# Performance work log

Hardware: AMD Instinct MI355X
Metric: run time of the kernel (lower is better)

Reference implementation:

```python
import jax, jax.numpy as jnp
import numpy as np

B, T, I, H, NSHIFT = 64, 1024, 128, 512, 32


def setup_inputs() -> dict:
    key = jax.random.key(0)
    ks = jax.random.split(key, 8)
    s_in = 1.0 / np.sqrt(I)
    s_h = 1.0 / np.sqrt(H)
    return {
        "x": jax.random.normal(ks[0], (B, T, I), dtype=jnp.float32),
        "W1": jax.random.uniform(ks[1], (I, H), minval=-s_in, maxval=s_in, dtype=jnp.float32),
        "b1": jax.random.uniform(ks[2], (H,), minval=-s_in, maxval=s_in, dtype=jnp.float32),
        "W_ih": jax.random.uniform(ks[3], (H, 4 * H), minval=-s_h, maxval=s_h, dtype=jnp.float32),
        "W_hh": jax.random.uniform(ks[4], (H, 4 * H), minval=-s_h, maxval=s_h, dtype=jnp.float32),
        "b_lstm": jax.random.uniform(ks[5], (4 * H,), minval=-s_h, maxval=s_h, dtype=jnp.float32),
        "Wo": jax.random.uniform(ks[6], (H, NSHIFT), minval=-s_h, maxval=s_h, dtype=jnp.float32),
        "bo": jax.random.uniform(ks[7], (NSHIFT,), minval=-s_h, maxval=s_h, dtype=jnp.float32),
    }


def _lstm_scan(xs, W_ih, W_hh, b, hidden):
    # xs: [T, B, H] (time-major for scan). Sine activation replaces tanh.
    Bsz = xs.shape[1]
    h0 = jnp.zeros((Bsz, hidden), dtype=xs.dtype)
    c0 = jnp.zeros((Bsz, hidden), dtype=xs.dtype)

    def step(carry, xt):
        h, c = carry
        gates = xt @ W_ih + h @ W_hh + b  # [B, 4H]
        i, f, g, o = jnp.split(gates, 4, axis=-1)
        i = jax.nn.sigmoid(i)
        f = jax.nn.sigmoid(f)
        g = jnp.sin(g)  # sine activation in place of tanh
        o = jax.nn.sigmoid(o)
        c_new = f * c + i * g
        h_new = o * jnp.sin(c_new)
        return (h_new, c_new), h_new

    (hT, cT), hs = jax.lax.scan(step, (h0, c0), xs)
    return hs, (hT, cT)


def reference(x, W1, b1, W_ih, W_hh, b_lstm, Wo, bo):
    # fc1: [B, T, I] -> [B, T, H]
    fc1_out = x @ W1 + b1
    xs = jnp.swapaxes(fc1_out, 0, 1)  # [T, B, H]
    hs, _ = _lstm_scan(xs, W_ih, W_hh, b_lstm, W_hh.shape[0])
    lstm_out = jnp.swapaxes(hs, 0, 1)  # [B, T, H]
    return lstm_out @ Wo + bo  # [B, T, n_shift]
```

## Files before the change

kernel.cpp:

```cpp
#include <hip/hip_runtime.h>


constexpr int Bb = 64;
constexpr int Tt = 1024;
constexpr int Ii = 128;
constexpr int Hh = 512;
constexpr int G4 = 2048;
constexpr int NS = 32;
constexpr int NG = 16;
constexpr int GW = 16;
constexpr int BPG = 4;

typedef _Float16 h2 __attribute__((ext_vector_type(2)));
typedef _Float16 h8 __attribute__((ext_vector_type(8)));
typedef float    f4 __attribute__((ext_vector_type(4)));
typedef unsigned int u32;
typedef u32 u32x2 __attribute__((ext_vector_type(2)));
typedef u32 u32x4 __attribute__((ext_vector_type(4)));

__device__ __forceinline__ float dot8(h8 w, h8 x, float acc) {
  h2 w0 = {w[0], w[1]}, w1 = {w[2], w[3]}, w2 = {w[4], w[5]}, w3 = {w[6], w[7]};
  h2 x0 = {x[0], x[1]}, x1 = {x[2], x[3]}, x2 = {x[4], x[5]}, x3 = {x[6], x[7]};
  acc = __builtin_amdgcn_fdot2(x0, w0, acc, false);
  acc = __builtin_amdgcn_fdot2(x1, w1, acc, false);
  acc = __builtin_amdgcn_fdot2(x2, w2, acc, false);
  acc = __builtin_amdgcn_fdot2(x3, w3, acc, false);
  return acc;
}

__device__ __forceinline__ float sigf(float x) { return 1.f / (1.f + __expf(-x)); }


__global__ void k_wc(const float* __restrict__ W1, const float* __restrict__ Wih,
                     const float* __restrict__ b1, const float* __restrict__ bl,
                     _Float16* __restrict__ Wc4, float* __restrict__ bias2) {
  const int j = blockIdx.x;
  const int i = threadIdx.x;
  __shared__ float col[Hh];
  __shared__ float part[128];
  for (int k = i; k < Hh; k += 128) col[k] = Wih[k * G4 + j];
  __syncthreads();
  float s = 0.f;
  for (int k = i; k < Hh; k += 128) s += b1[k] * col[k];
  part[i] = s;
  __syncthreads();
  if (i == 0) {
    float t = bl[j];
    for (int k = 0; k < 128; k++) t += part[k];
    bias2[j] = t;
  }
  float acc = 0.f;
  const float* w1r = W1 + i * Hh;
#pragma unroll 4
  for (int k = 0; k < Hh; k++) acc += w1r[k] * col[k];
  const int gate = j >> 9, r = j & 511, ss = r >> 5, u = r & 31;
  const int c128 = gate * 32 + u, cb = c128 >> 4, c = c128 & 15;
  const int lane = ((i >> 3) & 3) * 16 + c, ks4 = i >> 5, e = i & 7;
  Wc4[((ss * 8 + cb) * 4 + ks4) * 512 + lane * 8 + e] = (_Float16)acc;
}

__global__ void k_whh(const float* __restrict__ W, _Float16* __restrict__ W4) {
  const int id = blockIdx.x * 256 + threadIdx.x;
  const int lane = id & 63, ks = (id >> 6) & 15, cb = (id >> 10) & 7, ss = id >> 13;
  const int c = lane & 15, c128 = cb * 16 + c;
  const int gate = c128 >> 5, u = c128 & 31;
  const int colg = gate * 512 + ss * 32 + u;
  h8 o;
#pragma unroll
  for (int e = 0; e < 8; ++e)
    o[e] = (_Float16)W[(ks * 32 + (lane >> 4) * 8 + e) * G4 + colg];
  *(h8*)(W4 + ((ss * 8 + cb) * 16 + ks) * 512 + lane * 8) = o;
}

__global__ __launch_bounds__(512, 1) void k_scan(
    const float* __restrict__ x, const _Float16* __restrict__ Wc4,
    const float* __restrict__ bias2, const _Float16* __restrict__ Whh4,
    const float* __restrict__ Wo, const float* __restrict__ bo,
    float* __restrict__ out, char* __restrict__ hpub) {
  const int gid = blockIdx.x >> 4, ss = blockIdx.x & 15;
  const int tid = threadIdx.x;
  const int lane = tid & 63, wv = tid >> 6;
  const int l15 = lane & 15, l4 = lane >> 4;

  __shared__ __align__(16) char hls[2][16384];
  __shared__ __align__(16) char xws[4096];
  __shared__ __align__(16) char wots[32768];
  __shared__ float pre_s[2][2][4][4][33];
  __shared__ float gat_s[4][4][33];
  __shared__ float op_s[32][17];

  h8 bW[16], bC[4];
#pragma unroll
  for (int ks = 0; ks < 16; ++ks)
    bW[ks] = *(const h8*)(Whh4 + ((ss * 8 + wv) * 16 + ks) * 512 + lane * 8);
#pragma unroll
  for (int ks = 0; ks < 4; ++ks)
    bC[ks] = *(const h8*)(Wc4 + ((ss * 8 + wv) * 4 + ks) * 512 + lane * 8);

  const int b8 = tid >> 5, ml = tid & 31;
  const float bI = bias2[ss * 32 + ml],        bF = bias2[512 + ss * 32 + ml],
              bG = bias2[1024 + ss * 32 + ml], bO = bias2[1536 + ss * 32 + ml];
  const int nn = tid & 31, pp = tid >> 5;
  const float bor = (tid < NS) ? bo[tid] : 0.f;

#pragma unroll
  for (int q = 0; q < 2; ++q) {
    u32x4 z = {0, 0, 0, 0};
    *(u32x4*)(hls[0] + (q * 512 + tid) * 16) = z;
    *(u32x4*)(hls[1] + (q * 512 + tid) * 16) = z;
  }
  if (tid < 256) { u32x4 z = {0, 0, 0, 0}; *(u32x4*)(xws + tid * 16) = z; }
  for (int it = tid; it < Hh * NS; it += 512) {
    int k = it >> 5, n = it & 31;
    *(_Float16*)(wots + n * 1024 + ((2 * k) ^ ((n & 7) << 4))) = (_Float16)Wo[k * NS + n];
  }
  float c_ = 0.f;

  auto stage_x = [&](int t0) {
    if (tid < 128) {
      const int row = tid >> 4, cc = tid & 15;
      const float* src = x + ((size_t)(gid * BPG + (row & 3)) * Tt + t0 + (row >> 2)) * Ii + cc * 8;
      f4 s0 = *(const f4*)src, s1 = *(const f4*)(src + 4);
      h8 v = {(_Float16)s0[0], (_Float16)s0[1], (_Float16)s0[2], (_Float16)s0[3],
              (_Float16)s1[0], (_Float16)s1[1], (_Float16)s1[2], (_Float16)s1[3]};
      *(h8*)(xws + row * 256 + ((cc * 16) ^ ((row & 7) << 4))) = v;
    }
  };
  auto do_pregate = [&](int buf) {
    f4 pa = {0.f, 0.f, 0.f, 0.f};
#pragma unroll
    for (int ks = 0; ks < 4; ++ks) {
      const int row = l15;
      h8 a = *(const h8*)(xws + row * 256 + ((ks * 64 + l4 * 16) ^ ((row & 7) << 4)));
      pa = __builtin_amdgcn_mfma_f32_16x16x32_f16(a, bC[ks], pa, 0, 0, 0);
    }
    if (l4 < 2) {
      const int c128 = wv * 16 + l15, gam = c128 >> 5, u = c128 & 31;
#pragma unroll
      for (int e = 0; e < 4; ++e) {
        const int row = l4 * 4 + e;
        pre_s[buf][row >> 2][row & 3][gam][u] = pa[e];
      }
    }
  };
  auto op_part = [&](const char* hb) {
    if (ss < BPG) {
      float acc = 0.f;
#pragma unroll
      for (int q = 0; q < 4; ++q) {
        h8 w_ = *(const h8*)(wots + nn * 1024 + ((pp * 64 + q * 16) ^ ((nn & 7) << 4)));
        h8 hv = *(const h8*)(hb + ss * 1024 + ((pp * 64 + q * 16) ^ (ss << 4)));
        acc = dot8(w_, hv, acc);
      }
      op_s[nn][pp] = acc;
    }
  };

  stage_x(0);
  __syncthreads();
  do_pregate(0);

  int cur = 0;
#pragma unroll 1
  for (int t = 0; t < Tt; ++t) {
    char* const hpg = hpub + gid * 16384 + (t & 1) * 8192;
    const char* const hc = hls[cur];
    char* const hn_ = hls[cur ^ 1];
    {
      f4 g0 = {0.f, 0.f, 0.f, 0.f}, g1 = {0.f, 0.f, 0.f, 0.f};
#pragma unroll
      for (int ks = 0; ks < 16; ++ks) {
        const int row = l15;
        h8 a = *(const h8*)(hc + row * 1024 + ((ks * 64 + l4 * 16) ^ (row << 4)));
        if (ks & 1) g1 = __builtin_amdgcn_mfma_f32_16x16x32_f16(a, bW[ks], g1, 0, 0, 0);
        else        g0 = __builtin_amdgcn_mfma_f32_16x16x32_f16(a, bW[ks], g0, 0, 0, 0);
      }
      if (l4 == 0) {
        const int c128 = wv * 16 + l15, gam = c128 >> 5, u = c128 & 31;
#pragma unroll
        for (int e = 0; e < 4; ++e) gat_s[e][gam][u] = g0[e] + g1[e];
      }
    }
    __syncthreads();
    if (tid < 128) {
      const int ph = (t >> 1) & 1, tt = t & 1;
      float aI = gat_s[b8][0][ml] + pre_s[ph][tt][b8][0][ml] + bI;
      float aF = gat_s[b8][1][ml] + pre_s[ph][tt][b8][1][ml] + bF;
      float aG = gat_s[b8][2][ml] + pre_s[ph][tt][b8][2][ml] + bG;
      float aO = gat_s[b8][3][ml] + pre_s[ph][tt][b8][3][ml] + bO;
      float iv = sigf(aI), fv = sigf(aF), gv = __sinf(aG), ov = sigf(aO);
      c_ = fv * c_ + iv * gv;
      float hnv = ov * __sinf(c_);
      _Float16 hf = (_Float16)hnv;
      u32 pkt = (u32)__builtin_bit_cast(unsigned short, hf) | ((u32)(t + 1) << 16);
      u32* dst = (u32*)(hpg + ((size_t)(b8 * 512 + ss * 32 + ml)) * 4);
      asm volatile("global_store_dword %0, %1, off sc0 sc1" :: "v"(dst), "v"(pkt) : "memory");
    }
    if (!(t & 1)) { if (t <= 1020) stage_x(t + 2); }
    else if (t <= 1021) do_pregate(((t + 1) >> 1) & 1);
    if (t > 0) op_part(hc);
    {
      const u32* sp = (const u32*)(hpg + (size_t)tid * 16);
      const u32 want = (u32)(t + 1);
      u32x4 v;
      while (true) {
        asm volatile("global_load_dwordx4 %0, %1, off sc0 sc1\ns_waitcnt vmcnt(0)"
                     : "=v"(v) : "v"(sp) : "memory");
        if ((v[0] >> 16) == want && (v[1] >> 16) == want &&
            (v[2] >> 16) == want && (v[3] >> 16) == want) break;
      }
      __builtin_amdgcn_sched_barrier(0);
      u32x2 d = {(v[0] & 0xFFFFu) | (v[1] << 16), (v[2] & 0xFFFFu) | (v[3] << 16)};
      const int b = tid >> 7, k = tid & 127;
      *(u32x2*)(hn_ + b * 1024 + ((k * 8) ^ (b << 4))) = d;
    }
    __syncthreads();
    if (t > 0 && ss < BPG && tid < NS) {
      float s_ = bor;
#pragma unroll
      for (int p = 0; p < 16; ++p) s_ += op_s[tid][p];
      out[((size_t)(gid * BPG + ss) * Tt + (t - 1)) * NS + tid] = s_;
    }
    cur ^= 1;
  }
  op_part(hls[cur]);
  __syncthreads();
  if (ss < BPG && tid < NS) {
    float s_ = bor;
#pragma unroll
    for (int p = 0; p < 16; ++p) s_ += op_s[tid][p];
    out[((size_t)(gid * BPG + ss) * Tt + 1023) * NS + tid] = s_;
  }
}

extern "C" void kernel_launch(void* const* d_in, const int* in_sizes, int n_in,
                              void* d_out, int out_size, void* d_ws, size_t ws_size,
                              hipStream_t stream) {
  const float* x   = (const float*)d_in[0];
  const float* W1  = (const float*)d_in[1];
  const float* b1  = (const float*)d_in[2];
  const float* Wih = (const float*)d_in[3];
  const float* Whh = (const float*)d_in[4];
  const float* bl  = (const float*)d_in[5];
  const float* Wo  = (const float*)d_in[6];
  const float* bo  = (const float*)d_in[7];
  float* out = (float*)d_out;

  char* ws = (char*)d_ws;
  _Float16* Wc4   = (_Float16*)(ws);
  float*    bias2 = (float*)(ws + 524288);
  _Float16* Whh4  = (_Float16*)(ws + 532480);
  char*     hpub  = ws + 2629632;

  (void)hipMemsetAsync(hpub, 0, 262144, stream);
  k_wc<<<G4, 128, 0, stream>>>(W1, Wih, b1, bl, Wc4, bias2);
  k_whh<<<512, 256, 0, stream>>>(Whh, Whh4);
  k_scan<<<256, 512, 0, stream>>>(x, Wc4, bias2, Whh4, Wo, bo, out, hpub);
}
```

Before: 1.906 ms.

## Interleave gate columns per wave so cell update uses shuffles, not LDS barrier

Re-permutes the packed W_hh and fused input-weight layouts so that each wave's 16 MFMA output columns hold all four gates for four hidden units. The per-step gate results are gathered across lanes with shuffles and the cell update runs in the same wave, which removes the gat_s shared-memory round trip and one __syncthreads per time step. In exchange, only a quarter of the lanes do the cell math, extra shuffles are added, and the pre-gate LDS layout is re-indexed.

```diff
diff --git a/kernel.cpp b/kernel.cpp
--- a/kernel.cpp
+++ b/kernel.cpp
@@ -54,22 +54,22 @@
 #pragma unroll 4
   for (int k = 0; k < Hh; k++) acc += w1r[k] * col[k];
   const int gate = j >> 9, r = j & 511, ss = r >> 5, u = r & 31;
-  const int c128 = gate * 32 + u, cb = c128 >> 4, c = c128 & 15;
-  const int lane = ((i >> 3) & 3) * 16 + c, ks4 = i >> 5, e = i & 7;
-  Wc4[((ss * 8 + cb) * 4 + ks4) * 512 + lane * 8 + e] = (_Float16)acc;
+  const int wv = u >> 2, ul = u & 3;
+  const int l15 = ul * 4 + gate;
+  const int ks4 = i >> 5, l4 = (i >> 3) & 3, e = i & 7;
+  Wc4[((ss * 8 + wv) * 4 + ks4) * 512 + (l4 * 16 + l15) * 8 + e] = (_Float16)acc;
 }
 
 __global__ void k_whh(const float* __restrict__ W, _Float16* __restrict__ W4) {
   const int id = blockIdx.x * 256 + threadIdx.x;
-  const int lane = id & 63, ks = (id >> 6) & 15, cb = (id >> 10) & 7, ss = id >> 13;
-  const int c = lane & 15, c128 = cb * 16 + c;
-  const int gate = c128 >> 5, u = c128 & 31;
-  const int colg = gate * 512 + ss * 32 + u;
+  const int lane = id & 63, ks = (id >> 6) & 15, wv = (id >> 10) & 7, ss = id >> 13;
+  const int l15 = lane & 15, gate = l15 & 3, ul = l15 >> 2;
+  const int colg = gate * 512 + ss * 32 + wv * 4 + ul;
   h8 o;
 #pragma unroll
   for (int e = 0; e < 8; ++e)
     o[e] = (_Float16)W[(ks * 32 + (lane >> 4) * 8 + e) * G4 + colg];
-  *(h8*)(W4 + ((ss * 8 + cb) * 16 + ks) * 512 + lane * 8) = o;
+  *(h8*)(W4 + ((ss * 8 + wv) * 16 + ks) * 512 + lane * 8) = o;
 }
 
 __global__ __launch_bounds__(512, 1) void k_scan(
@@ -81,12 +81,15 @@
   const int tid = threadIdx.x;
   const int lane = tid & 63, wv = tid >> 6;
   const int l15 = lane & 15, l4 = lane >> 4;
+  const int ul = l15 >> 2;
+  const bool cellLane = ((l15 & 3) == 0);
+  const int unitW = wv * 4 + ul;
+  const int gunit = ss * 32 + unitW;
 
   __shared__ __align__(16) char hls[2][16384];
   __shared__ __align__(16) char xws[4096];
   __shared__ __align__(16) char wots[32768];
-  __shared__ float pre_s[2][2][4][4][33];
-  __shared__ float gat_s[4][4][33];
+  __shared__ float pre_s[2][2][4][4][36];
   __shared__ float op_s[32][17];
 
   h8 bW[16], bC[4];
@@ -97,9 +100,12 @@
   for (int ks = 0; ks < 4; ++ks)
     bC[ks] = *(const h8*)(Wc4 + ((ss * 8 + wv) * 4 + ks) * 512 + lane * 8);
 
-  const int b8 = tid >> 5, ml = tid & 31;
-  const float bI = bias2[ss * 32 + ml],        bF = bias2[512 + ss * 32 + ml],
-              bG = bias2[1024 + ss * 32 + ml], bO = bias2[1536 + ss * 32 + ml];
+  float bIr = 0.f, bFr = 0.f, bGr = 0.f, bOr = 0.f;
+  if (cellLane) {
+    bIr = bias2[gunit];        bFr = bias2[512 + gunit];
+    bGr = bias2[1024 + gunit]; bOr = bias2[1536 + gunit];
+  }
+  float c_ = 0.f;
   const int nn = tid & 31, pp = tid >> 5;
   const float bor = (tid < NS) ? bo[tid] : 0.f;
 
@@ -114,7 +120,6 @@
     int k = it >> 5, n = it & 31;
     *(_Float16*)(wots + n * 1024 + ((2 * k) ^ ((n & 7) << 4))) = (_Float16)Wo[k * NS + n];
   }
-  float c_ = 0.f;
 
   auto stage_x = [&](int t0) {
     if (tid < 128) {
@@ -135,12 +140,9 @@
       pa = __builtin_amdgcn_mfma_f32_16x16x32_f16(a, bC[ks], pa, 0, 0, 0);
     }
     if (l4 < 2) {
-      const int c128 = wv * 16 + l15, gam = c128 >> 5, u = c128 & 31;
-#pragma unroll
-      for (int e = 0; e < 4; ++e) {
-        const int row = l4 * 4 + e;
-        pre_s[buf][row >> 2][row & 3][gam][u] = pa[e];
-      }
+#pragma unroll
+      for (int e = 0; e < 4; ++e)
+        pre_s[buf][l4][e][l15 & 3][unitW] = pa[e];
     }
   };
   auto op_part = [&](const char* hb) {
@@ -166,34 +168,38 @@
     char* const hpg = hpub + gid * 16384 + (t & 1) * 8192;
     const char* const hc = hls[cur];
     char* const hn_ = hls[cur ^ 1];
-    {
-      f4 g0 = {0.f, 0.f, 0.f, 0.f}, g1 = {0.f, 0.f, 0.f, 0.f};
-#pragma unroll
-      for (int ks = 0; ks < 16; ++ks) {
-        const int row = l15;
-        h8 a = *(const h8*)(hc + row * 1024 + ((ks * 64 + l4 * 16) ^ (row << 4)));
-        if (ks & 1) g1 = __builtin_amdgcn_mfma_f32_16x16x32_f16(a, bW[ks], g1, 0, 0, 0);
-        else        g0 = __builtin_amdgcn_mfma_f32_16x16x32_f16(a, bW[ks], g0, 0, 0, 0);
-      }
-      if (l4 == 0) {
-        const int c128 = wv * 16 + l15, gam = c128 >> 5, u = c128 & 31;
-#pragma unroll
-        for (int e = 0; e < 4; ++e) gat_s[e][gam][u] = g0[e] + g1[e];
-      }
-    }
-    __syncthreads();
-    if (tid < 128) {
+    f4 g0 = {0.f, 0.f, 0.f, 0.f}, g1 = {0.f, 0.f, 0.f, 0.f};
+#pragma unroll
+    for (int ks = 0; ks < 16; ++ks) {
+      const int row = l15;
+      h8 a = *(const h8*)(hc + row * 1024 + ((ks * 64 + l4 * 16) ^ (row << 4)));
+      if (ks & 1) g1 = __builtin_amdgcn_mfma_f32_16x16x32_f16(a, bW[ks], g1, 0, 0, 0);
+      else        g0 = __builtin_amdgcn_mfma_f32_16x16x32_f16(a, bW[ks], g0, 0, 0, 0);
+    }
+    f4 gs;
+#pragma unroll
+    for (int e = 0; e < 4; ++e) gs[e] = g0[e] + g1[e];
+    float ag[4];
+#pragma unroll
+    for (int g = 0; g < 4; ++g) {
+      float t0 = __shfl(gs[0], l15 + g);
+      float t1 = __shfl(gs[1], l15 + g);
+      float t2 = __shfl(gs[2], l15 + g);
+      float t3 = __shfl(gs[3], l15 + g);
+      ag[g] = (l4 == 0) ? t0 : (l4 == 1) ? t1 : (l4 == 2) ? t2 : t3;
+    }
+    if (cellLane) {
       const int ph = (t >> 1) & 1, tt = t & 1;
-      float aI = gat_s[b8][0][ml] + pre_s[ph][tt][b8][0][ml] + bI;
-      float aF = gat_s[b8][1][ml] + pre_s[ph][tt][b8][1][ml] + bF;
-      float aG = gat_s[b8][2][ml] + pre_s[ph][tt][b8][2][ml] + bG;
-      float aO = gat_s[b8][3][ml] + pre_s[ph][tt][b8][3][ml] + bO;
+      float aI = ag[0] + pre_s[ph][tt][l4][0][unitW] + bIr;
+      float aF = ag[1] + pre_s[ph][tt][l4][1][unitW] + bFr;
+      float aG = ag[2] + pre_s[ph][tt][l4][2][unitW] + bGr;
+      float aO = ag[3] + pre_s[ph][tt][l4][3][unitW] + bOr;
       float iv = sigf(aI), fv = sigf(aF), gv = __sinf(aG), ov = sigf(aO);
       c_ = fv * c_ + iv * gv;
       float hnv = ov * __sinf(c_);
       _Float16 hf = (_Float16)hnv;
       u32 pkt = (u32)__builtin_bit_cast(unsigned short, hf) | ((u32)(t + 1) << 16);
-      u32* dst = (u32*)(hpg + ((size_t)(b8 * 512 + ss * 32 + ml)) * 4);
+      u32* dst = (u32*)(hpg + ((size_t)(l4 * 512 + gunit)) * 4);
       asm volatile("global_store_dword %0, %1, off sc0 sc1" :: "v"(dst), "v"(pkt) : "memory");
     }
     if (!(t & 1)) { if (t <= 1020) stage_x(t + 2); }
```

Result: slower. 2.852 ms (+49.6%).
